# Optimization experiments

Measured on AMD Instinct MI355X. Metric: run time of the kernel, lower is better.

Reference implementation:

```python
import jax, jax.numpy as jnp
import numpy as np

U, I, K = 50000, 30000, 64
D0, D1 = 768, 128
N_INTER = 1_000_000
N_LAYERS = 3
BATCH = 4096
EPS = 1e-12


def setup_inputs() -> dict:
    key = jax.random.key(0)
    k1, k2, k3, k4 = jax.random.split(key, 4)
    rng = np.random.default_rng(0)
    # bidirectional bipartite edges: user u <-> item node (U + i)
    u = rng.integers(0, U, size=N_INTER)
    i = rng.integers(0, I, size=N_INTER) + U
    src = np.concatenate([u, i])
    dst = np.concatenate([i, u])
    edge_index = jnp.asarray(np.stack([src, dst]), dtype=jnp.int32)  # [2, 2*N_INTER]
    return {
        "Gu": jax.random.normal(k1, (U, K), dtype=jnp.float32) * 0.1,
        "F0": jax.random.normal(k2, (I, D0), dtype=jnp.float32),
        "F1": jax.random.normal(k3, (I, D1), dtype=jnp.float32),
        "proj_w": jax.random.normal(k4, (D0 + D1, K), dtype=jnp.float32) * 0.03,
        "proj_b": jnp.zeros((K,), dtype=jnp.float32),
        "edge_index": edge_index,
        "user_idx": jnp.asarray(rng.integers(0, U, size=BATCH), dtype=jnp.int32),
        "item_idx": jnp.asarray(rng.integers(0, I, size=BATCH), dtype=jnp.int32),
    }


def _l2_normalize(x):
    # torch.nn.functional.normalize(p=2, dim=1) with eps clamp
    n = jnp.maximum(jnp.linalg.norm(x, axis=1, keepdims=True), EPS)
    return x / n


def reference(Gu, F0, F1, proj_w, proj_b, edge_index, user_idx, item_idx):
    N = U + I
    # concat aggregation: project concatenated multimodal features, L2-normalize rows
    F_proj = _l2_normalize(jnp.concatenate([F0, F1], axis=-1) @ proj_w + proj_b)
    x = jnp.concatenate([Gu, F_proj], axis=0)  # [N, K]

    src, dst = edge_index[0], edge_index[1]
    # gcn_norm without self-loops (LGConv default): D^{-1/2} A D^{-1/2}
    deg = jax.ops.segment_sum(jnp.ones(src.shape[0], dtype=x.dtype), dst, num_segments=N)
    dinv = jnp.where(deg > 0, jax.lax.rsqrt(jnp.maximum(deg, 1.0)), 0.0)
    norm = dinv[src] * dinv[dst]  # [E]

    layers = [x]
    for _ in range(N_LAYERS):
        msg = layers[-1][src] * norm[:, None]  # [E, K]
        layers.append(jax.ops.segment_sum(msg, dst, num_segments=N))

    all_emb = jnp.mean(jnp.stack(layers, axis=0), axis=0)  # layer-wise mean pooling
    gu, fi = all_emb[:U], all_emb[U:]

    # forward(): batched dot product between selected user/item embeddings
    xui = jnp.sum(gu[user_idx] * fi[item_idx], axis=1)  # [BATCH]
    return xui
```

## Files before the change

### kernel.cpp

```cpp
#include <hip/hip_runtime.h>
#include <hip/hip_bf16.h>

#define NU 50000
#define NI 30000
#define NN 80000
#define KDIM 64
#define DD0 768
#define DD1 128
#define DD 896

#define BROWS 128
#define NB (NN / BROWS)
#define CAPB 5120
#define CAP 96
#define REGION_BYTES 24576
#define ENTS_STRIDE (REGION_BYTES / 4)
#define CHUNK_PAIRS 4096

typedef __attribute__((ext_vector_type(8))) short short8v;
typedef __attribute__((ext_vector_type(4))) short short4v;
typedef __attribute__((ext_vector_type(4))) float float4v;
typedef unsigned short ushort_t;

struct bf16pair { short hi, lo; };

__device__ inline bf16pair f32_split_bf16(float v) {
    __hip_bfloat16 h = __float2bfloat16(v);
    float hf = __bfloat162float(h);
    __hip_bfloat16 l = __float2bfloat16(v - hf);
    bf16pair p;
    p.hi = *reinterpret_cast<short*>(&h);
    p.lo = *reinterpret_cast<short*>(&l);
    return p;
}

__device__ inline float bf16bits_to_f32(ushort_t u) {
    return __uint_as_float(((unsigned int)u) << 16);
}

__device__ inline ushort_t f32_to_bf16_rne(float f) {
    unsigned int u = __float_as_uint(f);
    unsigned int r = (u + 0x7FFFu + ((u >> 16) & 1u)) >> 16;
    return (ushort_t)r;
}

__global__ void wtcvt_kernel(const float* __restrict__ W,
                             short* __restrict__ WTh, short* __restrict__ WTl)
{
    const int i = blockIdx.x * 256 + threadIdx.x;
    if (i < DD * KDIM) {
        const int k = i >> 6, col = i & 63;
        const bf16pair p = f32_split_bf16(W[i]);
        WTh[col * DD + k] = p.hi;
        WTl[col * DD + k] = p.lo;
    }
}

__global__ __launch_bounds__(256) void proj_kernel(
    const float* __restrict__ F0, const float* __restrict__ F1,
    const short* __restrict__ WTh, const short* __restrict__ WTl,
    const float* __restrict__ b, const float* __restrict__ dinv,
    float* __restrict__ Fp, ushort_t* __restrict__ curS)
{
    __shared__ short Ah[32][72];
    __shared__ short Al[32][72];
    __shared__ short Bh[64][72];
    __shared__ short Bl[64][72];
    __shared__ float ssL[4][16];

    const int tid  = threadIdx.x;
    const int wv   = tid >> 6;
    const int lane = tid & 63;
    const int lr   = lane & 15;
    const int grp  = lane >> 4;
    const int rowBase = blockIdx.x * 32;
    const int rowGrp  = wv >> 1;
    const int colHalf = wv & 1;

    const int aR[2] = { (0*256+tid) >> 4, (1*256+tid) >> 4 };
    const int aK    = (tid & 15) * 4;
    const int bCol[2] = { (0*256+tid) >> 3, (1*256+tid) >> 3 };
    const int bK      = (tid & 7) * 8;

    float4   pA[2];
    short8v  pBh[2], pBl[2];

    auto loadChunk = [&](int c) {
        #pragma unroll
        for (int rep = 0; rep < 2; ++rep) {
            const int r = rowBase + aR[rep];
            float4 v = make_float4(0.f, 0.f, 0.f, 0.f);
            if (r < NI) {
                if (c < 12)
                    v = *(const float4*)&F0[(size_t)r * DD0 + c * 64 + aK];
                else
                    v = *(const float4*)&F1[(size_t)r * DD1 + (c - 12) * 64 + aK];
            }
            pA[rep] = v;
        }
        #pragma unroll
        for (int rep = 0; rep < 2; ++rep) {
            pBh[rep] = *(const short8v*)&WTh[(size_t)bCol[rep] * DD + c * 64 + bK];
            pBl[rep] = *(const short8v*)&WTl[(size_t)bCol[rep] * DD + c * 64 + bK];
        }
    };

    float4v acc[2] = {};

    loadChunk(0);
    for (int c = 0; c < 14; ++c) {
        #pragma unroll
        for (int rep = 0; rep < 2; ++rep) {
            const float4 v = pA[rep];
            const bf16pair p0 = f32_split_bf16(v.x);
            const bf16pair p1 = f32_split_bf16(v.y);
            const bf16pair p2 = f32_split_bf16(v.z);
            const bf16pair p3 = f32_split_bf16(v.w);
            short4v h4, l4;
            h4[0] = p0.hi; h4[1] = p1.hi; h4[2] = p2.hi; h4[3] = p3.hi;
            l4[0] = p0.lo; l4[1] = p1.lo; l4[2] = p2.lo; l4[3] = p3.lo;
            *(short4v*)&Ah[aR[rep]][aK] = h4;
            *(short4v*)&Al[aR[rep]][aK] = l4;
        }
        #pragma unroll
        for (int rep = 0; rep < 2; ++rep) {
            *(short8v*)&Bh[bCol[rep]][bK] = pBh[rep];
            *(short8v*)&Bl[bCol[rep]][bK] = pBl[rep];
        }
        if (c < 13) loadChunk(c + 1);
        __syncthreads();

        #pragma unroll
        for (int ks = 0; ks < 2; ++ks) {
            const int ko = ks * 32 + grp * 8;
            const short8v ah = *(const short8v*)&Ah[rowGrp * 16 + lr][ko];
            const short8v al = *(const short8v*)&Al[rowGrp * 16 + lr][ko];
            #pragma unroll
            for (int nt = 0; nt < 2; ++nt) {
                const int bc = colHalf * 32 + nt * 16 + lr;
                const short8v bh = *(const short8v*)&Bh[bc][ko];
                const short8v bl = *(const short8v*)&Bl[bc][ko];
                acc[nt] = __builtin_amdgcn_mfma_f32_16x16x32_bf16(ah, bh, acc[nt], 0, 0, 0);
                acc[nt] = __builtin_amdgcn_mfma_f32_16x16x32_bf16(ah, bl, acc[nt], 0, 0, 0);
                acc[nt] = __builtin_amdgcn_mfma_f32_16x16x32_bf16(al, bh, acc[nt], 0, 0, 0);
            }
        }
        __syncthreads();
    }

    float bias[2];
    #pragma unroll
    for (int nt = 0; nt < 2; ++nt) bias[nt] = b[colHalf * 32 + nt * 16 + lr];

    float y[2][4];
    #pragma unroll
    for (int i = 0; i < 4; ++i) {
        float s = 0.f;
        #pragma unroll
        for (int nt = 0; nt < 2; ++nt) {
            y[nt][i] = acc[nt][i] + bias[nt];
            s += y[nt][i] * y[nt][i];
        }
        s += __shfl_xor(s, 1);
        s += __shfl_xor(s, 2);
        s += __shfl_xor(s, 4);
        s += __shfl_xor(s, 8);
        if (lr == 0) ssL[wv][grp * 4 + i] = s;
    }
    __syncthreads();
    #pragma unroll
    for (int i = 0; i < 4; ++i) {
        const int rl = grp * 4 + i;
        const float ss = ssL[rowGrp * 2][rl] + ssL[rowGrp * 2 + 1][rl];
        const int r = rowBase + rowGrp * 16 + rl;
        if (r < NI) {
            const float inv = 1.0f / fmaxf(sqrtf(ss), 1e-12f);
            const float dv  = dinv[NU + r];
            #pragma unroll
            for (int nt = 0; nt < 2; ++nt) {
                const float o = y[nt][i] * inv;
                const int cc = colHalf * 32 + nt * 16 + lr;
                Fp[(size_t)(NU + r) * KDIM + cc] = o;
                curS[(size_t)(NU + r) * KDIM + cc] = f32_to_bf16_rne(o * dv);
            }
        }
    }
}

__global__ void userinit_kernel(const float* __restrict__ Gu,
                                const float* __restrict__ dinv,
                                ushort_t* __restrict__ curS)
{
    const int i = blockIdx.x * blockDim.x + threadIdx.x;
    if (i < NU * KDIM / 4) {
        const int row = i >> 4;
        const float dv = dinv[row];
        const float4 g = ((const float4*)Gu)[i];
        short4v s;
        s[0] = (short)f32_to_bf16_rne(g.x * dv);
        s[1] = (short)f32_to_bf16_rne(g.y * dv);
        s[2] = (short)f32_to_bf16_rne(g.z * dv);
        s[3] = (short)f32_to_bf16_rne(g.w * dv);
        *(short4v*)&curS[(size_t)i * 4] = s;
    }
}

__global__ __launch_bounds__(256) void part_kernel(
    const int* __restrict__ src, const int* __restrict__ dst,
    int* __restrict__ bcur, unsigned int* __restrict__ ents, int E2)
{
    __shared__ int bcntL[NB];
    __shared__ int bposL[NB];
    const int tid = threadIdx.x;
    const int pairBase = blockIdx.x * CHUNK_PAIRS;

    for (int i = tid; i < NB; i += 256) bcntL[i] = 0;
    __syncthreads();

    #pragma unroll
    for (int it = 0; it < CHUNK_PAIRS / 256; ++it) {
        const int p = pairBase + it * 256 + tid;
        if (p < E2) {
            const int u  = src[p];
            const int iF = dst[p];
            atomicAdd(&bcntL[iF >> 7], 1);
            atomicAdd(&bcntL[u  >> 7], 1);
        }
    }
    __syncthreads();

    for (int bkt = tid; bkt < NB; bkt += 256) {
        const int c = bcntL[bkt];
        bposL[bkt] = (c > 0) ? atomicAdd(&bcur[bkt], c) : 0;
        bcntL[bkt] = 0;
    }
    __syncthreads();

    #pragma unroll
    for (int it = 0; it < CHUNK_PAIRS / 256; ++it) {
        const int p = pairBase + it * 256 + tid;
        if (p < E2) {
            const int u  = src[p];
            const int iF = dst[p];
            {
                const int bkt = iF >> 7;
                const int k = bposL[bkt] + atomicAdd(&bcntL[bkt], 1);
                if (k < CAPB)
                    ents[(size_t)bkt * ENTS_STRIDE + k] =
                        ((unsigned int)(iF & 127) << 16) | (unsigned int)u;
            }
            {
                const int bkt = u >> 7;
                const int k = bposL[bkt] + atomicAdd(&bcntL[bkt], 1);
                if (k < CAPB)
                    ents[(size_t)bkt * ENTS_STRIDE + k] =
                        ((unsigned int)(u & 127) << 16) | (unsigned int)(iF - NU);
            }
        }
    }
}

__global__ __launch_bounds__(256) void toELL_kernel(
    const int* __restrict__ bcur, unsigned int* __restrict__ ents,
    ushort_t* __restrict__ col,
    int* __restrict__ cnt, float* __restrict__ dinv)
{
    __shared__ unsigned int eL[CAPB];
    __shared__ int curL[BROWS];
    const int bkt = blockIdx.x;
    const int tid = threadIdx.x;

    int n = bcur[bkt]; n = (n < CAPB) ? n : CAPB;
    const unsigned int* ep = ents + (size_t)bkt * ENTS_STRIDE;

    for (int j = tid; j < n; j += 256) eL[j] = ep[j];
    if (tid < BROWS) curL[tid] = 0;
    __syncthreads();

    const size_t rowB = (size_t)bkt * BROWS;
    for (int j = tid; j < n; j += 256) {
        const unsigned int e = eL[j];
        const int dl = (int)(e >> 16);
        const int slot = atomicAdd(&curL[dl], 1);
        if (slot < CAP)
            col[(rowB + dl) * CAP + slot] = (ushort_t)(e & 0xFFFFu);
    }
    __syncthreads();

    if (tid < BROWS) {
        int c = curL[tid];
        c = (c < CAP) ? c : CAP;
        const size_t row = rowB + tid;
        cnt[row]  = c;
        dinv[row] = (c > 0) ? rsqrtf((float)c) : 0.0f;
    }
}

__global__ __launch_bounds__(256) void pull_kernel(
    const ushort_t* __restrict__ curS, ushort_t* __restrict__ nxtS,
    const int* __restrict__ cnt,
    const ushort_t* __restrict__ col,
    const float* __restrict__ dinv,
    int rowStart, int nRows)
{
    const int wid = __builtin_amdgcn_readfirstlane(
        (int)((blockIdx.x * blockDim.x + threadIdx.x) >> 6));
    const int lane = threadIdx.x & 63;
    if (wid >= nRows) return;
    const int row = rowStart + wid;

    const unsigned int* cpd = (const unsigned int*)(col + (size_t)row * CAP);
    const int addB = (row < NU) ? NU : 0;
    const int n = cnt[row];

    float a0 = 0.f, a1 = 0.f, a2 = 0.f, a3 = 0.f;
    int j = 0;
    for (; j + 8 <= n; j += 8) {
        const uint4 cc = *(const uint4*)(cpd + (j >> 1));
        const int c0 = (int)(cc.x & 0xFFFFu) + addB;
        const int c1 = (int)(cc.x >> 16)     + addB;
        const int c2 = (int)(cc.y & 0xFFFFu) + addB;
        const int c3 = (int)(cc.y >> 16)     + addB;
        const int c4 = (int)(cc.z & 0xFFFFu) + addB;
        const int c5 = (int)(cc.z >> 16)     + addB;
        const int c6 = (int)(cc.w & 0xFFFFu) + addB;
        const int c7 = (int)(cc.w >> 16)     + addB;
        const float v0 = bf16bits_to_f32(curS[((size_t)c0 << 6) + lane]);
        const float v1 = bf16bits_to_f32(curS[((size_t)c1 << 6) + lane]);
        const float v2 = bf16bits_to_f32(curS[((size_t)c2 << 6) + lane]);
        const float v3 = bf16bits_to_f32(curS[((size_t)c3 << 6) + lane]);
        const float v4 = bf16bits_to_f32(curS[((size_t)c4 << 6) + lane]);
        const float v5 = bf16bits_to_f32(curS[((size_t)c5 << 6) + lane]);
        const float v6 = bf16bits_to_f32(curS[((size_t)c6 << 6) + lane]);
        const float v7 = bf16bits_to_f32(curS[((size_t)c7 << 6) + lane]);
        a0 += v0 + v4; a1 += v1 + v5; a2 += v2 + v6; a3 += v3 + v7;
    }
    for (; j < n; ++j) {
        const unsigned int d = cpd[j >> 1];
        const int c = (int)((j & 1) ? (d >> 16) : (d & 0xFFFFu)) + addB;
        a0 += bf16bits_to_f32(curS[((size_t)c << 6) + lane]);
    }

    const float dv = dinv[row];
    nxtS[((size_t)row << 6) + lane] =
        f32_to_bf16_rne(dv * dv * ((a0 + a1) + (a2 + a3)));
}

__device__ inline float row_acc(int row, float x0, int lane,
                                const ushort_t* __restrict__ S1,
                                const ushort_t* __restrict__ S2,
                                const int* __restrict__ cnt,
                                const ushort_t* __restrict__ col,
                                const float* __restrict__ dinv)
{
    const float dv  = dinv[row];
    const float rdv = (dv > 0.f) ? 1.0f / dv : 0.0f;
    const float s1 = bf16bits_to_f32(S1[((size_t)row << 6) + lane]);
    const float s2 = bf16bits_to_f32(S2[((size_t)row << 6) + lane]);

    const unsigned int* cpd = (const unsigned int*)(col + (size_t)row * CAP);
    const int addB = (row < NU) ? NU : 0;
    const int n = cnt[row];
    float a0 = 0.f, a1 = 0.f, a2 = 0.f, a3 = 0.f;
    int j = 0;
    for (; j + 8 <= n; j += 8) {
        const uint4 cc = *(const uint4*)(cpd + (j >> 1));
        const int c0 = (int)(cc.x & 0xFFFFu) + addB;
        const int c1 = (int)(cc.x >> 16)     + addB;
        const int c2 = (int)(cc.y & 0xFFFFu) + addB;
        const int c3 = (int)(cc.y >> 16)     + addB;
        const int c4 = (int)(cc.z & 0xFFFFu) + addB;
        const int c5 = (int)(cc.z >> 16)     + addB;
        const int c6 = (int)(cc.w & 0xFFFFu) + addB;
        const int c7 = (int)(cc.w >> 16)     + addB;
        const float v0 = bf16bits_to_f32(S2[((size_t)c0 << 6) + lane]);
        const float v1 = bf16bits_to_f32(S2[((size_t)c1 << 6) + lane]);
        const float v2 = bf16bits_to_f32(S2[((size_t)c2 << 6) + lane]);
        const float v3 = bf16bits_to_f32(S2[((size_t)c3 << 6) + lane]);
        const float v4 = bf16bits_to_f32(S2[((size_t)c4 << 6) + lane]);
        const float v5 = bf16bits_to_f32(S2[((size_t)c5 << 6) + lane]);
        const float v6 = bf16bits_to_f32(S2[((size_t)c6 << 6) + lane]);
        const float v7 = bf16bits_to_f32(S2[((size_t)c7 << 6) + lane]);
        a0 += v0 + v4; a1 += v1 + v5; a2 += v2 + v6; a3 += v3 + v7;
    }
    for (; j < n; ++j) {
        const unsigned int d = cpd[j >> 1];
        const int c = (int)((j & 1) ? (d >> 16) : (d & 0xFFFFu)) + addB;
        a0 += bf16bits_to_f32(S2[((size_t)c << 6) + lane]);
    }

    return x0 + (s1 + s2) * rdv + dv * ((a0 + a1) + (a2 + a3));
}

__global__ __launch_bounds__(256) void out_kernel(
    const float* __restrict__ Gu, const float* __restrict__ Fp,
    const ushort_t* __restrict__ S1, const ushort_t* __restrict__ S2,
    const int* __restrict__ cnt, const ushort_t* __restrict__ col,
    const float* __restrict__ dinv,
    const int* __restrict__ uidx, const int* __restrict__ iidx,
    float* __restrict__ out, int B)
{
    const int wid = __builtin_amdgcn_readfirstlane(
        (int)((blockIdx.x * blockDim.x + threadIdx.x) >> 6));
    const int lane = threadIdx.x & 63;
    if (wid >= B) return;
    const int u  = uidx[wid];
    const int rI = NU + iidx[wid];

    const float au = row_acc(u,  Gu[((size_t)u  << 6) + lane], lane,
                             S1, S2, cnt, col, dinv);
    const float ai = row_acc(rI, Fp[((size_t)rI << 6) + lane], lane,
                             S1, S2, cnt, col, dinv);
    float p = au * ai;
    #pragma unroll
    for (int m = 32; m >= 1; m >>= 1) p += __shfl_xor(p, m);
    if (lane == 0) out[wid] = p * (1.0f / 16.0f);
}

extern "C" void kernel_launch(void* const* d_in, const int* in_sizes, int n_in,
                              void* d_out, int out_size, void* d_ws, size_t ws_size,
                              hipStream_t stream)
{
    const float* Gu = (const float*)d_in[0];
    const float* F0 = (const float*)d_in[1];
    const float* F1 = (const float*)d_in[2];
    const float* W  = (const float*)d_in[3];
    const float* pb = (const float*)d_in[4];
    const int* edge = (const int*)d_in[5];
    const int* uidx = (const int*)d_in[6];
    const int* iidx = (const int*)d_in[7];
    const int E  = in_sizes[5] / 2;
    const int E2 = E / 2;
    const int B = in_sizes[6];
    const int* srcp = edge;
    const int* dstp = edge + E;

    const size_t XE = (size_t)NN * KDIM;
    float*    Fp    = (float*)d_ws;
    ushort_t* curA  = (ushort_t*)(Fp + XE);
    ushort_t* curB  = curA + XE;
    float*    dinv  = (float*)(curB + XE);
    int*      cnt   = (int*)(dinv + NN);
    int*      bcur  = cnt + NN;
    short*    WTh   = (short*)(bcur + NB);
    short*    WTl   = WTh + (size_t)KDIM * DD;
    ushort_t* col   = (ushort_t*)(WTl + (size_t)KDIM * DD);
    unsigned int* ents = (unsigned int*)col;

    (void)hipMemsetAsync(bcur, 0, NB * sizeof(int), stream);
    part_kernel<<<(E2 + CHUNK_PAIRS - 1) / CHUNK_PAIRS, 256, 0, stream>>>(
        srcp, dstp, bcur, ents, E2);
    toELL_kernel<<<NB, 256, 0, stream>>>(bcur, ents, col, cnt, dinv);

    wtcvt_kernel<<<(DD * KDIM + 255) / 256, 256, 0, stream>>>(W, WTh, WTl);

    userinit_kernel<<<(NU * KDIM / 4 + 255) / 256, 256, 0, stream>>>(
        Gu, dinv, curA);
    proj_kernel<<<(NI + 31) / 32, 256, 0, stream>>>(F0, F1, WTh, WTl, pb,
                                                    dinv, Fp, curA);

    const int gridU = (NU * 64 + 255) / 256;
    const int gridI = (NI * 64 + 255) / 256;
    pull_kernel<<<gridU, 256, 0, stream>>>(curA, curB, cnt, col, dinv, 0, NU);
    pull_kernel<<<gridI, 256, 0, stream>>>(curA, curB, cnt, col, dinv, NU, NI);
    pull_kernel<<<gridU, 256, 0, stream>>>(curB, curA, cnt, col, dinv, 0, NU);
    pull_kernel<<<gridI, 256, 0, stream>>>(curB, curA, cnt, col, dinv, NU, NI);

    out_kernel<<<(int)(((size_t)B * 64 + 255) / 256), 256, 0, stream>>>(
        Gu, Fp, curB, curA, cnt, col, dinv, uidx, iidx, (float*)d_out, B);
}
```

Baseline: 184.6 us.

## Split projection GEMM over K into two partial blocks with separate combine kernel

The projection GEMM now uses 64-row tiles with each wave covering all 64 output columns, and splits the 14 K-chunks across two blocks per row tile. Partial sums go to a workspace buffer. A new combine kernel adds the partials and bias, L2-normalizes each row and writes Fp and the scaled bf16 state. The aim is more parallelism and more reuse of the W tile per block, at the cost of an extra kernel launch and a round trip of partial sums through global memory.

After: 187.3 us. Within noise of the previous version (+1.5%).

```diff
diff --git a/kernel.cpp b/kernel.cpp
--- a/kernel.cpp
+++ b/kernel.cpp
@@ -56,38 +56,37 @@
     }
 }
 
-__global__ __launch_bounds__(256) void proj_kernel(
+__global__ __launch_bounds__(256) void projk_kernel(
     const float* __restrict__ F0, const float* __restrict__ F1,
     const short* __restrict__ WTh, const short* __restrict__ WTl,
-    const float* __restrict__ b, const float* __restrict__ dinv,
-    float* __restrict__ Fp, ushort_t* __restrict__ curS)
-{
-    __shared__ short Ah[32][72];
-    __shared__ short Al[32][72];
+    float* __restrict__ Ppart)
+{
+    __shared__ short Ah[64][72];
+    __shared__ short Al[64][72];
     __shared__ short Bh[64][72];
     __shared__ short Bl[64][72];
-    __shared__ float ssL[4][16];
 
     const int tid  = threadIdx.x;
     const int wv   = tid >> 6;
     const int lane = tid & 63;
     const int lr   = lane & 15;
     const int grp  = lane >> 4;
-    const int rowBase = blockIdx.x * 32;
-    const int rowGrp  = wv >> 1;
-    const int colHalf = wv & 1;
-
-    const int aR[2] = { (0*256+tid) >> 4, (1*256+tid) >> 4 };
+    const int rowBase = (blockIdx.x >> 1) * 64;
+    const int kz      = blockIdx.x & 1;
+    const int cBase   = kz * 7;
+
+    const int aR[4] = { (0*256+tid) >> 4, (1*256+tid) >> 4,
+                        (2*256+tid) >> 4, (3*256+tid) >> 4 };
     const int aK    = (tid & 15) * 4;
     const int bCol[2] = { (0*256+tid) >> 3, (1*256+tid) >> 3 };
     const int bK      = (tid & 7) * 8;
 
-    float4   pA[2];
+    float4   pA[4];
     short8v  pBh[2], pBl[2];
 
     auto loadChunk = [&](int c) {
         #pragma unroll
-        for (int rep = 0; rep < 2; ++rep) {
+        for (int rep = 0; rep < 4; ++rep) {
             const int r = rowBase + aR[rep];
             float4 v = make_float4(0.f, 0.f, 0.f, 0.f);
             if (r < NI) {
@@ -105,12 +104,12 @@
         }
     };
 
-    float4v acc[2] = {};
-
-    loadChunk(0);
-    for (int c = 0; c < 14; ++c) {
+    float4v acc[4] = {};
+
+    loadChunk(cBase);
+    for (int c = 0; c < 7; ++c) {
         #pragma unroll
-        for (int rep = 0; rep < 2; ++rep) {
+        for (int rep = 0; rep < 4; ++rep) {
             const float4 v = pA[rep];
             const bf16pair p0 = f32_split_bf16(v.x);
             const bf16pair p1 = f32_split_bf16(v.y);
@@ -127,19 +126,18 @@
             *(short8v*)&Bh[bCol[rep]][bK] = pBh[rep];
             *(short8v*)&Bl[bCol[rep]][bK] = pBl[rep];
         }
-        if (c < 13) loadChunk(c + 1);
+        if (c < 6) loadChunk(cBase + c + 1);
         __syncthreads();
 
         #pragma unroll
         for (int ks = 0; ks < 2; ++ks) {
             const int ko = ks * 32 + grp * 8;
-            const short8v ah = *(const short8v*)&Ah[rowGrp * 16 + lr][ko];
-            const short8v al = *(const short8v*)&Al[rowGrp * 16 + lr][ko];
+            const short8v ah = *(const short8v*)&Ah[wv * 16 + lr][ko];
+            const short8v al = *(const short8v*)&Al[wv * 16 + lr][ko];
             #pragma unroll
-            for (int nt = 0; nt < 2; ++nt) {
-                const int bc = colHalf * 32 + nt * 16 + lr;
-                const short8v bh = *(const short8v*)&Bh[bc][ko];
-                const short8v bl = *(const short8v*)&Bl[bc][ko];
+            for (int nt = 0; nt < 4; ++nt) {
+                const short8v bh = *(const short8v*)&Bh[nt * 16 + lr][ko];
+                const short8v bl = *(const short8v*)&Bl[nt * 16 + lr][ko];
                 acc[nt] = __builtin_amdgcn_mfma_f32_16x16x32_bf16(ah, bh, acc[nt], 0, 0, 0);
                 acc[nt] = __builtin_amdgcn_mfma_f32_16x16x32_bf16(ah, bl, acc[nt], 0, 0, 0);
                 acc[nt] = __builtin_amdgcn_mfma_f32_16x16x32_bf16(al, bh, acc[nt], 0, 0, 0);
@@ -148,43 +146,40 @@
         __syncthreads();
     }
 
-    float bias[2];
-    #pragma unroll
-    for (int nt = 0; nt < 2; ++nt) bias[nt] = b[colHalf * 32 + nt * 16 + lr];
-
-    float y[2][4];
     #pragma unroll
     for (int i = 0; i < 4; ++i) {
-        float s = 0.f;
-        #pragma unroll
-        for (int nt = 0; nt < 2; ++nt) {
-            y[nt][i] = acc[nt][i] + bias[nt];
-            s += y[nt][i] * y[nt][i];
-        }
-        s += __shfl_xor(s, 1);
-        s += __shfl_xor(s, 2);
-        s += __shfl_xor(s, 4);
-        s += __shfl_xor(s, 8);
-        if (lr == 0) ssL[wv][grp * 4 + i] = s;
-    }
-    __syncthreads();
-    #pragma unroll
-    for (int i = 0; i < 4; ++i) {
-        const int rl = grp * 4 + i;
-        const float ss = ssL[rowGrp * 2][rl] + ssL[rowGrp * 2 + 1][rl];
-        const int r = rowBase + rowGrp * 16 + rl;
+        const int r = rowBase + wv * 16 + 4 * grp + i;
         if (r < NI) {
-            const float inv = 1.0f / fmaxf(sqrtf(ss), 1e-12f);
-            const float dv  = dinv[NU + r];
             #pragma unroll
-            for (int nt = 0; nt < 2; ++nt) {
-                const float o = y[nt][i] * inv;
-                const int cc = colHalf * 32 + nt * 16 + lr;
-                Fp[(size_t)(NU + r) * KDIM + cc] = o;
-                curS[(size_t)(NU + r) * KDIM + cc] = f32_to_bf16_rne(o * dv);
-            }
-        }
-    }
+            for (int nt = 0; nt < 4; ++nt)
+                Ppart[((size_t)kz * NI + r) * KDIM + nt * 16 + lr] = acc[nt][i];
+        }
+    }
+}
+
+__global__ __launch_bounds__(256) void projcomb_kernel(
+    const float* __restrict__ Ppart, const float* __restrict__ b,
+    const float* __restrict__ dinv,
+    float* __restrict__ Fp, ushort_t* __restrict__ curS)
+{
+    const int wid  = (blockIdx.x * blockDim.x + threadIdx.x) >> 6;
+    const int lane = threadIdx.x & 63;
+    if (wid >= NI) return;
+    const float y = Ppart[(size_t)wid * KDIM + lane]
+                  + Ppart[((size_t)NI + wid) * KDIM + lane]
+                  + b[lane];
+    float ss = y * y;
+    ss += __shfl_xor(ss, 1);
+    ss += __shfl_xor(ss, 2);
+    ss += __shfl_xor(ss, 4);
+    ss += __shfl_xor(ss, 8);
+    ss += __shfl_xor(ss, 16);
+    ss += __shfl_xor(ss, 32);
+    const float inv = 1.0f / fmaxf(sqrtf(ss), 1e-12f);
+    const float dv  = dinv[NU + wid];
+    const float o = y * inv;
+    Fp[((size_t)(NU + wid)) * KDIM + lane] = o;
+    curS[((size_t)(NU + wid)) * KDIM + lane] = f32_to_bf16_rne(o * dv);
 }
 
 __global__ void userinit_kernel(const float* __restrict__ Gu,
@@ -446,6 +441,7 @@
     short*    WTl   = WTh + (size_t)KDIM * DD;
     ushort_t* col   = (ushort_t*)(WTl + (size_t)KDIM * DD);
     unsigned int* ents = (unsigned int*)col;
+    float*    Ppart = (float*)(col + (size_t)NB * (REGION_BYTES / 2));
 
     (void)hipMemsetAsync(bcur, 0, NB * sizeof(int), stream);
     part_kernel<<<(E2 + CHUNK_PAIRS - 1) / CHUNK_PAIRS, 256, 0, stream>>>(
@@ -454,10 +450,13 @@
 
     wtcvt_kernel<<<(DD * KDIM + 255) / 256, 256, 0, stream>>>(W, WTh, WTl);
 
+    projk_kernel<<<((NI + 63) / 64) * 2, 256, 0, stream>>>(F0, F1, WTh, WTl,
+                                                           Ppart);
+    projcomb_kernel<<<(NI * 64 + 255) / 256, 256, 0, stream>>>(
+        Ppart, pb, dinv, Fp, curA);
+
     userinit_kernel<<<(NU * KDIM / 4 + 255) / 256, 256, 0, stream>>>(
         Gu, dinv, curA);
-    proj_kernel<<<(NI + 31) / 32, 256, 0, stream>>>(F0, F1, WTh, WTl, pb,
-                                                    dinv, Fp, curA);
 
     const int gridU = (NU * 64 + 255) / 256;
     const int gridI = (NI * 64 + 255) / 256;
```
